# Kernel tuning notes

Hardware: AMD Instinct MI355X
Metric: run time of the kernel (lower is better)

The kernel has to match this reference:

```python
import jax, jax.numpy as jnp
import numpy as np

B, C, K = 128, 32, 128


def setup_inputs() -> dict:
    key = jax.random.key(0)
    k1, k2, k3, k4, k5 = jax.random.split(key, 5)
    x = jax.random.normal(k1, (B, 1, K, K), dtype=jnp.float32)
    # Conv2d(1, C, (1, K)) weight -> effectively [C, K] over the column axis
    w_col = jax.random.normal(k2, (C, K), dtype=jnp.float32) * (1.0 / np.sqrt(K))
    b_col = jax.random.normal(k3, (C,), dtype=jnp.float32) * 0.01
    # Conv2d(1, C, (K, 1)) weight -> effectively [C, K] over the row axis
    w_row = jax.random.normal(k4, (C, K), dtype=jnp.float32) * (1.0 / np.sqrt(K))
    b_row = jax.random.normal(k5, (C,), dtype=jnp.float32) * 0.01
    return {"x": x, "w_col": w_col, "b_col": b_col, "w_row": w_row, "b_row": b_row}


def reference(x, w_col, b_col, w_row, b_row):
    xs = x[:, 0]  # [B, K, K]
    # conv_column: kernel (1, K) contracts the column axis j -> [B, C, K] (rows i)
    col = jnp.einsum("bij,cj->bci", xs, w_col) + b_col[None, :, None]
    # conv_row: kernel (K, 1) contracts the row axis i -> [B, C, K] (cols j)
    row = jnp.einsum("bij,ci->bcj", xs, w_row) + b_row[None, :, None]
    # Tiling conv_row to [B,C,K,K] (identical rows) and conv_column to
    # [B,C,K,K] (identical columns) and matmul-ing yields, for every (i, j):
    #   out[b,c,i,j] = sum_k row[b,c,k] * col[b,c,k]
    # i.e. a per-(b,c) scalar broadcast over the K x K plane.
    s = jnp.einsum("bck,bck->bc", row, col)  # [B, C]
    return jnp.broadcast_to(s[:, :, None, None], (x.shape[0], w_col.shape[0], K, K))
```

## Files before the change

### kernel.cpp

```cpp
#include <hip/hip_runtime.h>
#include <hip/hip_bf16.h>


constexpr int KDIM = 128;
constexpr int CDIM = 32;

__device__ __forceinline__ int swz_word(int row, int col) {
    return (row << 7) | ((((col >> 2) ^ ((row >> 2) & 7)) << 2) | (col & 3));
}

__global__ __launch_bounds__(512) void fused_kernel(
    const float* __restrict__ x,
    const float* __restrict__ w_col, const float* __restrict__ b_col,
    const float* __restrict__ w_row, const float* __restrict__ b_row,
    float* __restrict__ out)
{
    __shared__ __align__(16) float xs[KDIM * KDIM];
    __shared__ __align__(16) float xt[KDIM * KDIM];
    __shared__ float4 wu4[KDIM][4];
    __shared__ float4 wc4[KDIM][4];

    const int bid  = blockIdx.x;
    const int xcd  = bid & 7;
    const int idx  = bid >> 3;
    const int b    = xcd * 16 + (idx >> 1);
    const int ch   = idx & 1;
    const int C0   = ch * 16;
    const int tid  = threadIdx.x;
    const int w    = tid >> 6;
    const int lane = tid & 63;

    {
        const int i = tid & 127;
        const int g = tid >> 7;
        wu4[i][g] = make_float4(w_row[(C0 + 4 * g + 0) * KDIM + i],
                                w_row[(C0 + 4 * g + 1) * KDIM + i],
                                w_row[(C0 + 4 * g + 2) * KDIM + i],
                                w_row[(C0 + 4 * g + 3) * KDIM + i]);
        wc4[i][g] = make_float4(w_col[(C0 + 4 * g + 0) * KDIM + i],
                                w_col[(C0 + 4 * g + 1) * KDIM + i],
                                w_col[(C0 + 4 * g + 2) * KDIM + i],
                                w_col[(C0 + 4 * g + 3) * KDIM + i]);
    }

    const float4* xsrc = reinterpret_cast<const float4*>(x + (size_t)b * KDIM * KDIM);
    const int tj  = tid & 31;
    const int ti0 = tid >> 5;
    #pragma unroll
    for (int it = 0; it < 2; ++it) {
        const int ti = ti0 + 16 * it;
        const float4 r0 = xsrc[(4 * ti + 0) * 32 + tj];
        const float4 r1 = xsrc[(4 * ti + 1) * 32 + tj];
        const float4 r2 = xsrc[(4 * ti + 2) * 32 + tj];
        const float4 r3 = xsrc[(4 * ti + 3) * 32 + tj];
        *reinterpret_cast<float4*>(&xs[(4 * ti + 0) * KDIM + 4 * tj]) = r0;
        *reinterpret_cast<float4*>(&xs[(4 * ti + 1) * KDIM + 4 * tj]) = r1;
        *reinterpret_cast<float4*>(&xs[(4 * ti + 2) * KDIM + 4 * tj]) = r2;
        *reinterpret_cast<float4*>(&xs[(4 * ti + 3) * KDIM + 4 * tj]) = r3;
        *reinterpret_cast<float4*>(&xt[swz_word(4 * tj + 0, 4 * ti)]) =
            make_float4(r0.x, r1.x, r2.x, r3.x);
        *reinterpret_cast<float4*>(&xt[swz_word(4 * tj + 1, 4 * ti)]) =
            make_float4(r0.y, r1.y, r2.y, r3.y);
        *reinterpret_cast<float4*>(&xt[swz_word(4 * tj + 2, 4 * ti)]) =
            make_float4(r0.z, r1.z, r2.z, r3.z);
        *reinterpret_cast<float4*>(&xt[swz_word(4 * tj + 3, 4 * ti)]) =
            make_float4(r0.w, r1.w, r2.w, r3.w);
    }
    __syncthreads();

    const int role = w >> 2;
    const int g    = w & 3;
    const int kq   = lane & 31;
    const int ih   = lane >> 5;
    const int k0   = 4 * kq;

    float a[4][4] = {{0,0,0,0},{0,0,0,0},{0,0,0,0},{0,0,0,0}};

    if (role == 0) {
        #pragma unroll 8
        for (int ii = 0; ii < 64; ++ii) {
            const int i = ih * 64 + ii;
            const float4 xv = *reinterpret_cast<const float4*>(&xs[i * KDIM + k0]);
            const float4 wq = wu4[i][g];
            #pragma unroll
            for (int cc = 0; cc < 4; ++cc) {
                const float ww = (&wq.x)[cc];
                a[cc][0] = fmaf(ww, xv.x, a[cc][0]);
                a[cc][1] = fmaf(ww, xv.y, a[cc][1]);
                a[cc][2] = fmaf(ww, xv.z, a[cc][2]);
                a[cc][3] = fmaf(ww, xv.w, a[cc][3]);
            }
        }
    } else {
        #pragma unroll 8
        for (int ii = 0; ii < 64; ++ii) {
            const int j = ih * 64 + ii;
            const float4 tv = *reinterpret_cast<const float4*>(&xt[swz_word(j, k0)]);
            const float4 wq = wc4[j][g];
            #pragma unroll
            for (int cc = 0; cc < 4; ++cc) {
                const float ww = (&wq.x)[cc];
                a[cc][0] = fmaf(ww, tv.x, a[cc][0]);
                a[cc][1] = fmaf(ww, tv.y, a[cc][1]);
                a[cc][2] = fmaf(ww, tv.z, a[cc][2]);
                a[cc][3] = fmaf(ww, tv.w, a[cc][3]);
            }
        }
    }

    #pragma unroll
    for (int cc = 0; cc < 4; ++cc)
        #pragma unroll
        for (int q = 0; q < 4; ++q)
            a[cc][q] += __shfl_xor(a[cc][q], 32);

    __syncthreads();

    if (lane < 32) {
        float* ex = xs + role * 2048;
        #pragma unroll
        for (int cc = 0; cc < 4; ++cc) {
            *reinterpret_cast<float4*>(&ex[(4 * g + cc) * KDIM + k0]) =
                make_float4(a[cc][0], a[cc][1], a[cc][2], a[cc][3]);
        }
    }
    __syncthreads();

    {
        const int cg  = tid >> 5;
        const int kq2 = tid & 31;
        const float4 uu = *reinterpret_cast<const float4*>(&xs[cg * KDIM + 4 * kq2]);
        const float4 vv = *reinterpret_cast<const float4*>(&xs[2048 + cg * KDIM + 4 * kq2]);
        const int c = C0 + cg;
        const float br = b_row[c];
        const float bc = b_col[c];
        float p = (uu.x + br) * (vv.x + bc) + (uu.y + br) * (vv.y + bc)
                + (uu.z + br) * (vv.z + bc) + (uu.w + br) * (vv.w + bc);
        #pragma unroll
        for (int off = 1; off < 32; off <<= 1) p += __shfl_xor(p, off, 32);
        if (kq2 == 0) xt[cg] = p;
    }
    __syncthreads();

    float4* out4 = reinterpret_cast<float4*>(out);
    #pragma unroll
    for (int cl = 0; cl < 16; ++cl) {
        const float val = xt[cl];
        float4 v4;
        v4.x = v4.y = v4.z = v4.w = val;
        float4* o = out4 + (size_t)(b * CDIM + C0 + cl) * 4096;
        #pragma unroll
        for (int r = 0; r < 8; ++r) {
            o[tid + 512 * r] = v4;
        }
    }
}

extern "C" void kernel_launch(void* const* d_in, const int* in_sizes, int n_in,
                              void* d_out, int out_size, void* d_ws, size_t ws_size,
                              hipStream_t stream) {
    const float* x     = (const float*)d_in[0];
    const float* w_col = (const float*)d_in[1];
    const float* b_col = (const float*)d_in[2];
    const float* w_row = (const float*)d_in[3];
    const float* b_row = (const float*)d_in[4];
    float* out = (float*)d_out;

    fused_kernel<<<256, 512, 0, stream>>>(x, w_col, b_col, w_row, b_row, out);
}
```

Baseline: 52.03 us.

## Load x straight to LDS with XOR swizzle and drop transposed copy

The x tile now goes from global memory straight into LDS with async global_load_lds, using an XOR-swizzled chunk layout, instead of a register round-trip that also built a second transposed copy. The column-conv branch reads the swizzled tile column-wise in 4-row groups, with w_col stored in its natural layout. This halves LDS use and removes the transpose writes and their bank conflicts. The kernel is still dominated by the large broadcast output write, so the effect on total time may be small.

```diff
diff --git a/kernel.cpp b/kernel.cpp
--- a/kernel.cpp
+++ b/kernel.cpp
@@ -4,10 +4,6 @@
 
 constexpr int KDIM = 128;
 constexpr int CDIM = 32;
-
-__device__ __forceinline__ int swz_word(int row, int col) {
-    return (row << 7) | ((((col >> 2) ^ ((row >> 2) & 7)) << 2) | (col & 3));
-}
 
 __global__ __launch_bounds__(512) void fused_kernel(
     const float* __restrict__ x,
@@ -16,9 +12,9 @@
     float* __restrict__ out)
 {
     __shared__ __align__(16) float xs[KDIM * KDIM];
-    __shared__ __align__(16) float xt[KDIM * KDIM];
     __shared__ float4 wu4[KDIM][4];
-    __shared__ float4 wc4[KDIM][4];
+    __shared__ float4 wcv[16][32];
+    __shared__ float  s_b[16];
 
     const int bid  = blockIdx.x;
     const int xcd  = bid & 7;
@@ -30,6 +26,20 @@
     const int w    = tid >> 6;
     const int lane = tid & 63;
 
+    const float* xg = x + (size_t)b * KDIM * KDIM;
+    {
+        const int cb = w * 64 + lane;
+        #pragma unroll
+        for (int e = 0; e < 8; ++e) {
+            const int c    = cb + 512 * e;
+            const int row  = c >> 5;
+            const int scol = (c & 31) ^ ((c >> 7) & 31);
+            __builtin_amdgcn_global_load_lds(
+                (const __attribute__((address_space(1))) unsigned int*)(xg + row * KDIM + 4 * scol),
+                (__attribute__((address_space(3))) unsigned int*)(&xs[4 * c]),
+                16, 0, 0);
+        }
+    }
     {
         const int i = tid & 127;
         const int g = tid >> 7;
@@ -37,34 +47,9 @@
                                 w_row[(C0 + 4 * g + 1) * KDIM + i],
                                 w_row[(C0 + 4 * g + 2) * KDIM + i],
                                 w_row[(C0 + 4 * g + 3) * KDIM + i]);
-        wc4[i][g] = make_float4(w_col[(C0 + 4 * g + 0) * KDIM + i],
-                                w_col[(C0 + 4 * g + 1) * KDIM + i],
-                                w_col[(C0 + 4 * g + 2) * KDIM + i],
-                                w_col[(C0 + 4 * g + 3) * KDIM + i]);
-    }
-
-    const float4* xsrc = reinterpret_cast<const float4*>(x + (size_t)b * KDIM * KDIM);
-    const int tj  = tid & 31;
-    const int ti0 = tid >> 5;
-    #pragma unroll
-    for (int it = 0; it < 2; ++it) {
-        const int ti = ti0 + 16 * it;
-        const float4 r0 = xsrc[(4 * ti + 0) * 32 + tj];
-        const float4 r1 = xsrc[(4 * ti + 1) * 32 + tj];
-        const float4 r2 = xsrc[(4 * ti + 2) * 32 + tj];
-        const float4 r3 = xsrc[(4 * ti + 3) * 32 + tj];
-        *reinterpret_cast<float4*>(&xs[(4 * ti + 0) * KDIM + 4 * tj]) = r0;
-        *reinterpret_cast<float4*>(&xs[(4 * ti + 1) * KDIM + 4 * tj]) = r1;
-        *reinterpret_cast<float4*>(&xs[(4 * ti + 2) * KDIM + 4 * tj]) = r2;
-        *reinterpret_cast<float4*>(&xs[(4 * ti + 3) * KDIM + 4 * tj]) = r3;
-        *reinterpret_cast<float4*>(&xt[swz_word(4 * tj + 0, 4 * ti)]) =
-            make_float4(r0.x, r1.x, r2.x, r3.x);
-        *reinterpret_cast<float4*>(&xt[swz_word(4 * tj + 1, 4 * ti)]) =
-            make_float4(r0.y, r1.y, r2.y, r3.y);
-        *reinterpret_cast<float4*>(&xt[swz_word(4 * tj + 2, 4 * ti)]) =
-            make_float4(r0.z, r1.z, r2.z, r3.z);
-        *reinterpret_cast<float4*>(&xt[swz_word(4 * tj + 3, 4 * ti)]) =
-            make_float4(r0.w, r1.w, r2.w, r3.w);
+        const int c16 = tid >> 5;
+        const int jc  = tid & 31;
+        wcv[c16][jc] = *reinterpret_cast<const float4*>(&w_col[(C0 + c16) * KDIM + 4 * jc]);
     }
     __syncthreads();
 
@@ -72,15 +57,15 @@
     const int g    = w & 3;
     const int kq   = lane & 31;
     const int ih   = lane >> 5;
-    const int k0   = 4 * kq;
 
     float a[4][4] = {{0,0,0,0},{0,0,0,0},{0,0,0,0},{0,0,0,0}};
 
     if (role == 0) {
-        #pragma unroll 8
+        #pragma unroll 4
         for (int ii = 0; ii < 64; ++ii) {
-            const int i = ih * 64 + ii;
-            const float4 xv = *reinterpret_cast<const float4*>(&xs[i * KDIM + k0]);
+            const int i     = ih * 64 + ii;
+            const int chunk = kq ^ ((i >> 2) & 31);
+            const float4 xv = *reinterpret_cast<const float4*>(&xs[i * KDIM + 4 * chunk]);
             const float4 wq = wu4[i][g];
             #pragma unroll
             for (int cc = 0; cc < 4; ++cc) {
@@ -92,18 +77,26 @@
             }
         }
     } else {
-        #pragma unroll 8
-        for (int ii = 0; ii < 64; ++ii) {
-            const int j = ih * 64 + ii;
-            const float4 tv = *reinterpret_cast<const float4*>(&xt[swz_word(j, k0)]);
-            const float4 wq = wc4[j][g];
+        #pragma unroll 2
+        for (int jj = 0; jj < 16; ++jj) {
+            const int jcol = ih * 16 + jj;
+            float4 tv[4];
+            #pragma unroll
+            for (int r = 0; r < 4; ++r) {
+                const int row   = 4 * kq + r;
+                const int chunk = jcol ^ kq;
+                tv[r] = *reinterpret_cast<const float4*>(&xs[row * KDIM + 4 * chunk]);
+            }
             #pragma unroll
             for (int cc = 0; cc < 4; ++cc) {
-                const float ww = (&wq.x)[cc];
-                a[cc][0] = fmaf(ww, tv.x, a[cc][0]);
-                a[cc][1] = fmaf(ww, tv.y, a[cc][1]);
-                a[cc][2] = fmaf(ww, tv.z, a[cc][2]);
-                a[cc][3] = fmaf(ww, tv.w, a[cc][3]);
+                const float4 wq = wcv[4 * g + cc][jcol];
+                #pragma unroll
+                for (int r = 0; r < 4; ++r) {
+                    a[cc][r] = fmaf(wq.x, tv[r].x, a[cc][r]);
+                    a[cc][r] = fmaf(wq.y, tv[r].y, a[cc][r]);
+                    a[cc][r] = fmaf(wq.z, tv[r].z, a[cc][r]);
+                    a[cc][r] = fmaf(wq.w, tv[r].w, a[cc][r]);
+                }
             }
         }
     }
@@ -120,7 +113,7 @@
         float* ex = xs + role * 2048;
         #pragma unroll
         for (int cc = 0; cc < 4; ++cc) {
-            *reinterpret_cast<float4*>(&ex[(4 * g + cc) * KDIM + k0]) =
+            *reinterpret_cast<float4*>(&ex[(4 * g + cc) * KDIM + 4 * kq]) =
                 make_float4(a[cc][0], a[cc][1], a[cc][2], a[cc][3]);
         }
     }
@@ -138,14 +131,14 @@
                 + (uu.z + br) * (vv.z + bc) + (uu.w + br) * (vv.w + bc);
         #pragma unroll
         for (int off = 1; off < 32; off <<= 1) p += __shfl_xor(p, off, 32);
-        if (kq2 == 0) xt[cg] = p;
+        if (kq2 == 0) s_b[cg] = p;
     }
     __syncthreads();
 
     float4* out4 = reinterpret_cast<float4*>(out);
     #pragma unroll
     for (int cl = 0; cl < 16; ++cl) {
-        const float val = xt[cl];
+        const float val = s_b[cl];
         float4 v4;
         v4.x = v4.y = v4.z = v4.w = val;
         float4* o = out4 + (size_t)(b * CDIM + C0 + cl) * 4096;
```

Result: no change. 52.49 us (+0.9%).
